# Kernel tuning notes

Measured on AMD Instinct MI355X. Metric: run time of the kernel, lower is better.

Reference implementation:

```python
import jax, jax.numpy as jnp
import numpy as np

B_IMG, B_CAP, T_CAP, D = 64, 64, 64, 1024
H = D // 8          # CBN MLP bottleneck (k=8)
T_IMG = 36          # fixed number of image regions; cap_embed truncated to this
EPS = 1e-5          # BatchNorm eps
GAMMA = 10.0        # softmax gate temperature (norm_output=True)


def _l2norm(x, axis=-1):
    return x / jnp.linalg.norm(x, axis=axis, keepdims=True)


def setup_inputs() -> dict:
    key = jax.random.key(0)
    ks = jax.random.split(key, 8)
    s1 = 1.0 / np.sqrt(D)
    s2 = 1.0 / np.sqrt(H)
    return {
        "img_embed": jax.random.normal(ks[0], (B_IMG, T_IMG, D), jnp.float32),
        "cap_embed": jax.random.normal(ks[1], (B_CAP, T_CAP, D), jnp.float32),
        "lens": jax.random.randint(ks[2], (B_CAP,), 1, T_CAP + 1).astype(jnp.int32),
        # CondBatchNorm1d gamma/beta predictor MLPs: Linear(D,H)->ReLU->Linear(H,D)
        "Wg1": jax.random.normal(ks[3], (D, H), jnp.float32) * s1,
        "bg1": jnp.zeros((H,), jnp.float32),
        "Wg2": jax.random.normal(ks[4], (H, D), jnp.float32) * s2,
        "bg2": jnp.zeros((D,), jnp.float32),
        "Wb1": jax.random.normal(ks[5], (D, H), jnp.float32) * s1,
        "bb1": jnp.zeros((H,), jnp.float32),
        "Wb2": jax.random.normal(ks[6], (H, D), jnp.float32) * s2,
        "bb2": jnp.zeros((D,), jnp.float32),
    }


def reference(img_embed, cap_embed, lens, Wg1, bg1, Wg2, bg2, Wb1, bb1, Wb2, bb2):
    # permute to channels-first and truncate captions to 36 timesteps
    cap = jnp.transpose(cap_embed, (0, 2, 1))[:, :, :T_IMG]   # (Bc, D, 36)
    img = jnp.transpose(img_embed, (0, 2, 1))                 # (Bi, D, 36)
    img_repr = img.mean(-1)                                   # (Bi, D)

    # BatchNorm1d (affine=False), training-mode batch stats over (Bc, T) per channel.
    # cap is identical across the original per-image loop, so normalize once.
    mu = cap.mean(axis=(0, 2), keepdims=True)
    var = cap.var(axis=(0, 2), keepdims=True)
    xn = (cap - mu) / jnp.sqrt(var + EPS)                     # (Bc, D, 36)

    # condition-dependent gamma/beta per image (CBN: 1 + delta_gamma)
    gam = 1.0 + (jax.nn.relu(img_repr @ Wg1 + bg1) @ Wg2 + bg2)   # (Bi, D)
    bet = jax.nn.relu(img_repr @ Wb1 + bb1) @ Wb2 + bb2           # (Bi, D)

    # vectorized over the original Python loop: (Bi, Bc, D, 36)
    txt = gam[:, None, :, None] * xn[None] + bet[:, None, :, None]
    mask = jax.nn.softmax(txt * GAMMA, axis=-1)               # gate over time axis
    txt_vec = (mask * txt).mean(-1)                           # (Bi, Bc, D)

    txt_vec = _l2norm(txt_vec, -1)
    img_vec = _l2norm(img_repr, -1)                           # (Bi, D)
    sims = jnp.einsum("id,ibd->ib", img_vec, txt_vec)        # (Bi, Bc)
    return sims
```

## Files before the change

kernel.cpp:

```cpp
#include <hip/hip_runtime.h>
#include <hip/hip_bf16.h>

#define BI 64
#define BC 64
#define TCAP 64
#define D 1024
#define H 128
#define TIMG 36

__global__ __launch_bounds__(256) void k_pre(const float* __restrict__ img,
                                             const float* __restrict__ cap,
                                             const float* __restrict__ Wg1,
                                             const float* __restrict__ Wb1,
                                             float* __restrict__ repr,
                                             float* __restrict__ ivec,
                                             float* __restrict__ part,
                                             float* __restrict__ W1T) {
    int blk = blockIdx.x, tid = threadIdx.x;
    if (blk < 64) {
        int i = blk;
        const float4* base = (const float4*)(img + (size_t)i * TIMG * D);
        float4 s = {0.f, 0.f, 0.f, 0.f};
        for (int t = 0; t < TIMG; ++t) {
            float4 v = base[t * 256 + tid];
            s.x += v.x; s.y += v.y; s.z += v.z; s.w += v.w;
        }
        s.x *= (1.f / 36.f); s.y *= (1.f / 36.f); s.z *= (1.f / 36.f); s.w *= (1.f / 36.f);
        ((float4*)(repr + (size_t)i * D))[tid] = s;
        float local = s.x * s.x + s.y * s.y + s.z * s.z + s.w * s.w;
        for (int off = 32; off; off >>= 1) local += __shfl_xor(local, off);
        __shared__ float red[4];
        int wave = tid >> 6;
        if ((tid & 63) == 0) red[wave] = local;
        __syncthreads();
        float inv = rsqrtf(red[0] + red[1] + red[2] + red[3]);
        float4 o = {s.x * inv, s.y * inv, s.z * inv, s.w * inv};
        ((float4*)(ivec + (size_t)i * D))[tid] = o;
    } else if (blk < 128) {
        int b = blk - 64;
        const float4* base = (const float4*)(cap + (size_t)b * TCAP * D);
        float4 s = {0.f, 0.f, 0.f, 0.f}, ss = {0.f, 0.f, 0.f, 0.f};
        for (int t = 0; t < TIMG; ++t) {
            float4 v = base[t * 256 + tid];
            s.x += v.x; s.y += v.y; s.z += v.z; s.w += v.w;
            ss.x = fmaf(v.x, v.x, ss.x); ss.y = fmaf(v.y, v.y, ss.y);
            ss.z = fmaf(v.z, v.z, ss.z); ss.w = fmaf(v.w, v.w, ss.w);
        }
        ((float4*)(part + b * 2048))[tid] = s;
        ((float4*)(part + b * 2048 + 1024))[tid] = ss;
    } else {
        __shared__ float tile[64][65];
        int idx = blk - 128;
        int bx = idx & 15, by = (idx >> 4) & 1, bz = idx >> 5;
        const float* W = bz ? Wb1 : Wg1;
        int d0 = bx * 64, c0 = by * 64;
        int lane = tid & 63, w = tid >> 6;
#pragma unroll
        for (int k = 0; k < 16; ++k) {
            int dl = k * 4 + w;
            tile[dl][lane] = W[(size_t)(d0 + dl) * H + c0 + lane];
        }
        __syncthreads();
#pragma unroll
        for (int k = 0; k < 16; ++k) {
            int cl = k * 4 + w;
            W1T[(size_t)(bz * 128 + c0 + cl) * D + d0 + lane] = tile[lane][cl];
        }
    }
}

__global__ __launch_bounds__(256) void k_mid(const float* __restrict__ part,
                                             const float* __restrict__ repr,
                                             const float* __restrict__ W1T,
                                             const float* __restrict__ bg1,
                                             const float* __restrict__ bb1,
                                             float* __restrict__ mu,
                                             float* __restrict__ istd,
                                             float* __restrict__ hid) {
    int blk = blockIdx.x, tid = threadIdx.x;
    if (blk < 4) {
        int d = blk * 256 + tid;
        float s = 0.f, ss = 0.f;
        for (int g = 0; g < BC; ++g) {
            s += part[g * 2048 + d];
            ss += part[g * 2048 + 1024 + d];
        }
        const float invN = 1.f / 2304.f;
        float m = s * invN;
        float v = ss * invN - m * m;
        mu[d] = m;
        istd[d] = rsqrtf(v + 1e-5f);
    } else {
        int o = (blk - 4) * 4 + (tid >> 6);
        int lane = tid & 63;
        int i = o >> 8, c = o & 255;
        const float4* r = (const float4*)(repr + (size_t)i * D);
        const float4* w = (const float4*)(W1T + (size_t)c * D);
        float acc = 0.f;
#pragma unroll
        for (int k = 0; k < 4; ++k) {
            float4 rv = r[k * 64 + lane];
            float4 wv = w[k * 64 + lane];
            acc = fmaf(rv.x, wv.x, acc);
            acc = fmaf(rv.y, wv.y, acc);
            acc = fmaf(rv.z, wv.z, acc);
            acc = fmaf(rv.w, wv.w, acc);
        }
        for (int off = 32; off; off >>= 1) acc += __shfl_xor(acc, off);
        if (lane == 0) {
            float b = (c < 128) ? bg1[c] : bb1[c - 128];
            hid[o] = fmaxf(acc + b, 0.f);
        }
    }
}

__global__ __launch_bounds__(256) void k_out(const float* __restrict__ hid,
                                             const float* __restrict__ Wg2, const float* __restrict__ bg2,
                                             const float* __restrict__ Wb2, const float* __restrict__ bb2,
                                             float* __restrict__ gam, float* __restrict__ bet) {
    int i = blockIdx.x >> 1;
    int d2 = (blockIdx.x & 1) * 256 + threadIdx.x;
    __shared__ float h[256];
    h[threadIdx.x] = hid[i * 256 + threadIdx.x];
    __syncthreads();
    float2 g = ((const float2*)bg2)[d2];
    float2 bb = ((const float2*)bb2)[d2];
#pragma unroll 4
    for (int hh = 0; hh < H; ++hh) {
        float2 wg = ((const float2*)(Wg2 + (size_t)hh * D))[d2];
        float2 wb = ((const float2*)(Wb2 + (size_t)hh * D))[d2];
        float hg = h[hh], hb = h[128 + hh];
        g.x = fmaf(hg, wg.x, g.x);
        g.y = fmaf(hg, wg.y, g.y);
        bb.x = fmaf(hb, wb.x, bb.x);
        bb.y = fmaf(hb, wb.y, bb.y);
    }
    float2 go = {1.f + g.x, 1.f + g.y};
    ((float2*)(gam + (size_t)i * D))[d2] = go;
    ((float2*)(bet + (size_t)i * D))[d2] = bb;
}

__global__ __launch_bounds__(512) void k_main(const float* __restrict__ cap,
                                              const float* __restrict__ mu,
                                              const float* __restrict__ istd,
                                              const float* __restrict__ gam,
                                              const float* __restrict__ bet,
                                              const float* __restrict__ ivec,
                                              float* __restrict__ out) {
    int b = blockIdx.x, ig = blockIdx.y, tid = threadIdx.x;
    const float2* base = (const float2*)(cap + (size_t)b * TCAP * D);
    float2 mu2 = ((const float2*)mu)[tid];
    float2 is2 = ((const float2*)istd)[tid];
    const float A = 14.4269504089f;
    const float INV = 0.0693147180560f;

    float a0[8], a1[8], c0[8], c1[8];
    float sw0[8], sw1[8], sxa0[8], sxa1[8];
#pragma unroll
    for (int k = 0; k < 8; ++k) {
        int i = ig * 8 + k;
        float2 g = ((const float2*)(gam + (size_t)i * D))[tid];
        float2 be = ((const float2*)(bet + (size_t)i * D))[tid];
        a0[k] = A * g.x;
        a1[k] = A * g.y;
        c0[k] = A * (be.x - 6.f);
        c1[k] = A * (be.y - 6.f);
        sw0[k] = 0.f; sw1[k] = 0.f; sxa0[k] = 0.f; sxa1[k] = 0.f;
    }
#pragma unroll 4
    for (int t = 0; t < TIMG; ++t) {
        float2 cp = base[t * 512 + tid];
        float x0 = (cp.x - mu2.x) * is2.x;
        float x1 = (cp.y - mu2.y) * is2.y;
#pragma unroll
        for (int k = 0; k < 8; ++k) {
            float arg0 = fmaf(a0[k], x0, c0[k]);
            float e0 = __builtin_amdgcn_exp2f(arg0);
            sw0[k] += e0;
            sxa0[k] = fmaf(e0, arg0, sxa0[k]);
            float arg1 = fmaf(a1[k], x1, c1[k]);
            float e1 = __builtin_amdgcn_exp2f(arg1);
            sw1[k] += e1;
            sxa1[k] = fmaf(e1, arg1, sxa1[k]);
        }
    }
    __shared__ float redS[8][8], redD[8][8];
    int wave = tid >> 6;
#pragma unroll
    for (int k = 0; k < 8; ++k) {
        int i = ig * 8 + k;
        float2 iv = ((const float2*)(ivec + (size_t)i * D))[tid];
        float tv0 = fmaf(INV, sxa0[k] / sw0[k], 6.f);
        float tv1 = fmaf(INV, sxa1[k] / sw1[k], 6.f);
        float ss = tv0 * tv0 + tv1 * tv1;
        float sd = iv.x * tv0 + iv.y * tv1;
        for (int off = 32; off; off >>= 1) {
            ss += __shfl_xor(ss, off);
            sd += __shfl_xor(sd, off);
        }
        if ((tid & 63) == 0) { redS[k][wave] = ss; redD[k][wave] = sd; }
    }
    __syncthreads();
    if (tid < 64) {
        int k = tid >> 3, w = tid & 7;
        float s = redS[k][w], d = redD[k][w];
#pragma unroll
        for (int off = 1; off < 8; off <<= 1) {
            s += __shfl_xor(s, off);
            d += __shfl_xor(d, off);
        }
        if (w == 0) {
            int i = ig * 8 + k;
            out[i * BC + b] = d * rsqrtf(s);
        }
    }
}

extern "C" void kernel_launch(void* const* d_in, const int* in_sizes, int n_in,
                              void* d_out, int out_size, void* d_ws, size_t ws_size,
                              hipStream_t stream) {
    const float* img = (const float*)d_in[0];
    const float* cap = (const float*)d_in[1];
    const float* Wg1 = (const float*)d_in[3];
    const float* bg1 = (const float*)d_in[4];
    const float* Wg2 = (const float*)d_in[5];
    const float* bg2 = (const float*)d_in[6];
    const float* Wb1 = (const float*)d_in[7];
    const float* bb1 = (const float*)d_in[8];
    const float* Wb2 = (const float*)d_in[9];
    const float* bb2 = (const float*)d_in[10];

    float* ws = (float*)d_ws;
    float* repr = ws;
    float* ivec = ws + 65536;
    float* gam  = ws + 131072;
    float* bet  = ws + 196608;
    float* mu   = ws + 262144;
    float* istd = ws + 263168;
    float* part = ws + 264192;
    float* W1T  = ws + 395264;
    float* hid  = ws + 657408;
    float* out = (float*)d_out;

    k_pre<<<dim3(192), dim3(256), 0, stream>>>(img, cap, Wg1, Wb1, repr, ivec, part, W1T);
    k_mid<<<dim3(4100), dim3(256), 0, stream>>>(part, repr, W1T, bg1, bb1, mu, istd, hid);
    k_out<<<dim3(128), dim3(256), 0, stream>>>(hid, Wg2, bg2, Wb2, bb2, gam, bet);
    k_main<<<dim3(BC, 8), dim3(512), 0, stream>>>(cap, mu, istd, gam, bet, ivec, out);
}
```

Measured before the change: 55.44 us.

## Fuse CBN MLP hidden and output layers into one per-image kernel

```diff
diff --git a/kernel.cpp b/kernel.cpp
--- a/kernel.cpp
+++ b/kernel.cpp
@@ -69,75 +69,77 @@
     }
 }
 
-__global__ __launch_bounds__(256) void k_mid(const float* __restrict__ part,
+__global__ __launch_bounds__(256) void k_mlp(const float* __restrict__ part,
                                              const float* __restrict__ repr,
                                              const float* __restrict__ W1T,
                                              const float* __restrict__ bg1,
                                              const float* __restrict__ bb1,
+                                             const float* __restrict__ Wg2, const float* __restrict__ bg2,
+                                             const float* __restrict__ Wb2, const float* __restrict__ bb2,
                                              float* __restrict__ mu,
                                              float* __restrict__ istd,
-                                             float* __restrict__ hid) {
+                                             float* __restrict__ gam, float* __restrict__ bet) {
     int blk = blockIdx.x, tid = threadIdx.x;
     if (blk < 4) {
-        int d = blk * 256 + tid;
-        float s = 0.f, ss = 0.f;
+        if (blk > 0) return;
+        const float4* p4 = (const float4*)part;
+        float4 s = {0.f, 0.f, 0.f, 0.f}, q = {0.f, 0.f, 0.f, 0.f};
         for (int g = 0; g < BC; ++g) {
-            s += part[g * 2048 + d];
-            ss += part[g * 2048 + 1024 + d];
+            float4 a4 = p4[g * 512 + tid];
+            float4 b4 = p4[g * 512 + 256 + tid];
+            s.x += a4.x; s.y += a4.y; s.z += a4.z; s.w += a4.w;
+            q.x += b4.x; q.y += b4.y; q.z += b4.z; q.w += b4.w;
         }
         const float invN = 1.f / 2304.f;
-        float m = s * invN;
-        float v = ss * invN - m * m;
-        mu[d] = m;
-        istd[d] = rsqrtf(v + 1e-5f);
-    } else {
-        int o = (blk - 4) * 4 + (tid >> 6);
-        int lane = tid & 63;
-        int i = o >> 8, c = o & 255;
-        const float4* r = (const float4*)(repr + (size_t)i * D);
-        const float4* w = (const float4*)(W1T + (size_t)c * D);
+        float4 m = {s.x * invN, s.y * invN, s.z * invN, s.w * invN};
+        float4 v = {q.x * invN - m.x * m.x, q.y * invN - m.y * m.y,
+                    q.z * invN - m.z * m.z, q.w * invN - m.w * m.w};
+        ((float4*)mu)[tid] = m;
+        float4 ist = {rsqrtf(v.x + 1e-5f), rsqrtf(v.y + 1e-5f),
+                      rsqrtf(v.z + 1e-5f), rsqrtf(v.w + 1e-5f)};
+        ((float4*)istd)[tid] = ist;
+        return;
+    }
+    int i = blk - 4;
+    int lane = tid & 63, wave = tid >> 6;
+    __shared__ float h[256];
+    const float4* r4 = (const float4*)(repr + (size_t)i * D);
+    float4 rv0 = r4[lane], rv1 = r4[64 + lane], rv2 = r4[128 + lane], rv3 = r4[192 + lane];
+    for (int j = 0; j < 64; ++j) {
+        int cc = wave * 64 + j;
+        const float4* w4 = (const float4*)(W1T + (size_t)cc * D);
+        float4 w0 = w4[lane], w1 = w4[64 + lane], w2 = w4[128 + lane], w3 = w4[192 + lane];
         float acc = 0.f;
-#pragma unroll
-        for (int k = 0; k < 4; ++k) {
-            float4 rv = r[k * 64 + lane];
-            float4 wv = w[k * 64 + lane];
-            acc = fmaf(rv.x, wv.x, acc);
-            acc = fmaf(rv.y, wv.y, acc);
-            acc = fmaf(rv.z, wv.z, acc);
-            acc = fmaf(rv.w, wv.w, acc);
-        }
+        acc = fmaf(rv0.x, w0.x, acc); acc = fmaf(rv0.y, w0.y, acc);
+        acc = fmaf(rv0.z, w0.z, acc); acc = fmaf(rv0.w, w0.w, acc);
+        acc = fmaf(rv1.x, w1.x, acc); acc = fmaf(rv1.y, w1.y, acc);
+        acc = fmaf(rv1.z, w1.z, acc); acc = fmaf(rv1.w, w1.w, acc);
+        acc = fmaf(rv2.x, w2.x, acc); acc = fmaf(rv2.y, w2.y, acc);
+        acc = fmaf(rv2.z, w2.z, acc); acc = fmaf(rv2.w, w2.w, acc);
+        acc = fmaf(rv3.x, w3.x, acc); acc = fmaf(rv3.y, w3.y, acc);
+        acc = fmaf(rv3.z, w3.z, acc); acc = fmaf(rv3.w, w3.w, acc);
         for (int off = 32; off; off >>= 1) acc += __shfl_xor(acc, off);
         if (lane == 0) {
-            float b = (c < 128) ? bg1[c] : bb1[c - 128];
-            hid[o] = fmaxf(acc + b, 0.f);
-        }
-    }
-}
-
-__global__ __launch_bounds__(256) void k_out(const float* __restrict__ hid,
-                                             const float* __restrict__ Wg2, const float* __restrict__ bg2,
-                                             const float* __restrict__ Wb2, const float* __restrict__ bb2,
-                                             float* __restrict__ gam, float* __restrict__ bet) {
-    int i = blockIdx.x >> 1;
-    int d2 = (blockIdx.x & 1) * 256 + threadIdx.x;
-    __shared__ float h[256];
-    h[threadIdx.x] = hid[i * 256 + threadIdx.x];
+            float b1v = (cc < 128) ? bg1[cc] : bb1[cc - 128];
+            h[cc] = fmaxf(acc + b1v, 0.f);
+        }
+    }
     __syncthreads();
-    float2 g = ((const float2*)bg2)[d2];
-    float2 bb = ((const float2*)bb2)[d2];
+    float4 g = ((const float4*)bg2)[tid];
+    float4 bv = ((const float4*)bb2)[tid];
 #pragma unroll 4
     for (int hh = 0; hh < H; ++hh) {
-        float2 wg = ((const float2*)(Wg2 + (size_t)hh * D))[d2];
-        float2 wb = ((const float2*)(Wb2 + (size_t)hh * D))[d2];
         float hg = h[hh], hb = h[128 + hh];
-        g.x = fmaf(hg, wg.x, g.x);
-        g.y = fmaf(hg, wg.y, g.y);
-        bb.x = fmaf(hb, wb.x, bb.x);
-        bb.y = fmaf(hb, wb.y, bb.y);
-    }
-    float2 go = {1.f + g.x, 1.f + g.y};
-    ((float2*)(gam + (size_t)i * D))[d2] = go;
-    ((float2*)(bet + (size_t)i * D))[d2] = bb;
+        float4 wg = ((const float4*)(Wg2 + (size_t)hh * D))[tid];
+        float4 wb = ((const float4*)(Wb2 + (size_t)hh * D))[tid];
+        g.x = fmaf(hg, wg.x, g.x); g.y = fmaf(hg, wg.y, g.y);
+        g.z = fmaf(hg, wg.z, g.z); g.w = fmaf(hg, wg.w, g.w);
+        bv.x = fmaf(hb, wb.x, bv.x); bv.y = fmaf(hb, wb.y, bv.y);
+        bv.z = fmaf(hb, wb.z, bv.z); bv.w = fmaf(hb, wb.w, bv.w);
+    }
+    float4 go = {1.f + g.x, 1.f + g.y, 1.f + g.z, 1.f + g.w};
+    ((float4*)(gam + (size_t)i * D))[tid] = go;
+    ((float4*)(bet + (size_t)i * D))[tid] = bv;
 }
 
 __global__ __launch_bounds__(512) void k_main(const float* __restrict__ cap,
@@ -239,11 +241,10 @@
     float* istd = ws + 263168;
     float* part = ws + 264192;
     float* W1T  = ws + 395264;
-    float* hid  = ws + 657408;
     float* out = (float*)d_out;
 
     k_pre<<<dim3(192), dim3(256), 0, stream>>>(img, cap, Wg1, Wb1, repr, ivec, part, W1T);
-    k_mid<<<dim3(4100), dim3(256), 0, stream>>>(part, repr, W1T, bg1, bb1, mu, istd, hid);
-    k_out<<<dim3(128), dim3(256), 0, stream>>>(hid, Wg2, bg2, Wb2, bb2, gam, bet);
+    k_mlp<<<dim3(68), dim3(256), 0, stream>>>(part, repr, W1T, bg1, bb1,
+                                              Wg2, bg2, Wb2, bb2, mu, istd, gam, bet);
     k_main<<<dim3(BC, 8), dim3(512), 0, stream>>>(cap, mu, istd, gam, bet, ivec, out);
 }
```

New measurement: 90.29 us. +62.9%, slower.
